# Performance work log

Measured on AMD Instinct MI355X. Metric: run time of the kernel, lower is better.

The kernel has to match this reference:

```python
import jax, jax.numpy as jnp
import numpy as np

EPS = 1e-12

def _normalize(x, axis=-1):
    # matches torch F.normalize: x / max(||x||, eps)
    n = jnp.sqrt(jnp.sum(x * x, axis=axis, keepdims=True))
    return x / jnp.maximum(n, EPS)

def setup_inputs() -> dict:
    key = jax.random.key(0)
    k1, k2, k3, k4, k5 = jax.random.split(key, 5)
    B, D, N = 65536, 512, 64
    feature = jax.random.normal(k1, (B, D), dtype=jnp.float32)
    target = jax.random.randint(k2, (B, N), 0, 2, dtype=jnp.int32)
    W = jax.random.normal(k3, (N, 2, D), dtype=jnp.float32) * 0.05
    b = jax.random.normal(k4, (N, 2), dtype=jnp.float32) * 0.01
    u = jax.random.normal(k5, (N, 2), dtype=jnp.float32)
    return {"feature": feature, "target": target, "W": W, "b": b, "u": u}

def reference(feature, target, W, b, u):
    # spectral norm, one power iteration per head (torch default n_power_iterations=1)
    v = _normalize(jnp.einsum('nod,no->nd', W, u))      # [N, D]
    u1 = _normalize(jnp.einsum('nod,nd->no', W, v))      # [N, 2]
    # u, v are buffers (no grad through them in torch)
    u_s = jax.lax.stop_gradient(u1)
    v_s = jax.lax.stop_gradient(v)
    sigma = jnp.einsum('no,nod,nd->n', u_s, W, v_s)      # [N]
    W_sn = W / sigma[:, None, None]
    # dropout in eval mode = identity; fused batched matmul over all heads
    pred = jnp.einsum('bd,nod->bno', feature, W_sn) + b[None]   # [B, N, 2]
    output = jnp.argmax(pred, axis=2)                           # [B, N]
    # CrossEntropyLoss with soft targets: class dim is dim=1 (nclass), as in torch code
    onehot = jax.nn.one_hot(target, 2, dtype=jnp.float32)       # [B, N, 2]
    logp = jax.nn.log_softmax(pred, axis=1)                     # softmax over nclass dim
    loss = jnp.mean(-jnp.sum(onehot * logp, axis=1))            # mean over B and the 2-dim
    return pred, output, loss
```

## Files before the change

### kernel.cpp

```cpp
#include <hip/hip_runtime.h>
#include <math.h>

typedef __bf16 bf16x8 __attribute__((ext_vector_type(8)));
typedef float  f32x4  __attribute__((ext_vector_type(4)));

#define BROWS 65536
#define DIM   512
#define NHEAD 64
#define NCOL  128

#define PRED_SZ  ((size_t)BROWS * NCOL)
#define ARG_BASE PRED_SZ
#define LOSS_IDX (PRED_SZ + (size_t)BROWS * NHEAD)
#define BF_OFF   ARG_BASE
#define PART_OFF (ARG_BASE + 1056 * (size_t)NHEAD)
#define FIX_ROWS 1088


__global__ __launch_bounds__(64) void spectral_kernel(
    const float* __restrict__ W, const float* __restrict__ u,
    __bf16* __restrict__ Bfrag)
{
    int n = blockIdx.x;
    int lane = threadIdx.x;

    const float* W0 = W + (size_t)n * 2 * DIM;
    const float* W1 = W0 + DIM;
    float u0 = u[2 * n], u1v = u[2 * n + 1];

    float w0[8], w1[8], vr[8];
    {
        float4 a0 = *(const float4*)(W0 + lane * 8);
        float4 a1 = *(const float4*)(W0 + lane * 8 + 4);
        float4 b0 = *(const float4*)(W1 + lane * 8);
        float4 b1 = *(const float4*)(W1 + lane * 8 + 4);
        w0[0]=a0.x; w0[1]=a0.y; w0[2]=a0.z; w0[3]=a0.w;
        w0[4]=a1.x; w0[5]=a1.y; w0[6]=a1.z; w0[7]=a1.w;
        w1[0]=b0.x; w1[1]=b0.y; w1[2]=b0.z; w1[3]=b0.w;
        w1[4]=b1.x; w1[5]=b1.y; w1[6]=b1.z; w1[7]=b1.w;
    }

    float ss = 0.f;
#pragma unroll
    for (int j = 0; j < 8; ++j) {
        vr[j] = fmaf(w0[j], u0, w1[j] * u1v);
        ss = fmaf(vr[j], vr[j], ss);
    }
#pragma unroll
    for (int m = 32; m >= 1; m >>= 1) ss += __shfl_xor(ss, m, 64);
    float inv_n = 1.f / fmaxf(sqrtf(ss), 1e-12f);

    float s0 = 0.f, s1 = 0.f;
#pragma unroll
    for (int j = 0; j < 8; ++j) {
        float v = vr[j] * inv_n;
        s0 = fmaf(w0[j], v, s0);
        s1 = fmaf(w1[j], v, s1);
    }
#pragma unroll
    for (int m = 32; m >= 1; m >>= 1) {
        s0 += __shfl_xor(s0, m, 64);
        s1 += __shfl_xor(s1, m, 64);
    }
    float nu = sqrtf(fmaf(s0, s0, s1 * s1));
    float inv_nu = 1.f / fmaxf(nu, 1e-12f);
    float sigma = fmaf(s0 * inv_nu, s0, (s1 * inv_nu) * s1);
    float inv_sigma = 1.f / sigma;

    int kc2 = lane >> 2;
    int q   = lane & 3;
#pragma unroll
    for (int o = 0; o < 2; ++o) {
        int col = 2 * n + o;
        int nt = col >> 4, cc = col & 15;
        bf16x8 hi;
#pragma unroll
        for (int j = 0; j < 8; ++j)
            hi[j] = (__bf16)((o ? w1[j] : w0[j]) * inv_sigma);
        *(bf16x8*)(Bfrag + (size_t)(kc2 * 8 + nt) * 512 + (q * 16 + cc) * 8) = hi;
    }
}

#define CVT8H(H, F0, F1) {            \
    H[0] = (__bf16)(F0).x; H[1] = (__bf16)(F0).y; \
    H[2] = (__bf16)(F0).z; H[3] = (__bf16)(F0).w; \
    H[4] = (__bf16)(F1).x; H[5] = (__bf16)(F1).y; \
    H[6] = (__bf16)(F1).z; H[7] = (__bf16)(F1).w; }

__device__ __forceinline__ void gld_lds16(const __bf16* g, __bf16* l) {
    __builtin_amdgcn_global_load_lds(
        (const __attribute__((address_space(1))) void*)g,
        (__attribute__((address_space(3))) void*)l, 16, 0, 0);
}

__global__ __launch_bounds__(1024, 4) void gemm_fused(
    const float* __restrict__ A, const int* __restrict__ target,
    const __bf16* __restrict__ Bfrag, const float* __restrict__ bias,
    float* __restrict__ pred, float* __restrict__ outArg,
    float* __restrict__ partials)
{
    __shared__ __bf16 Bs[32768];

    int tid  = threadIdx.x;
    int wave = tid >> 6;
    int lane = tid & 63;
    int q = lane >> 4;
    int c = lane & 15;
    int rowBase = blockIdx.x * 256 + wave * 16;

    f32x4 acc[8] = {};

    const float* ap = A + (size_t)(rowBase + c) * DIM + q * 8;
    float4 x0 = *(const float4*)(ap);
    float4 x1 = *(const float4*)(ap + 4);

#pragma unroll
    for (int half = 0; half < 2; ++half) {
        if (half) __syncthreads();
        {
            const __bf16* gB = Bfrag + (size_t)half * 32768
                             + (size_t)(wave * 4) * 512 + lane * 8;
            __bf16* lB = Bs + (size_t)(wave * 4) * 512;
#pragma unroll
            for (int t = 0; t < 4; ++t)
                gld_lds16(gB + t * 512, lB + t * 512);
        }
        __syncthreads();

#pragma unroll
        for (int kc = 0; kc < 8; ++kc) {
            float4 n0, n1;
            if (!(half == 1 && kc == 7)) {
                int kn = half * 256 + kc * 32 + 32;
                n0 = *(const float4*)(ap + kn);
                n1 = *(const float4*)(ap + kn + 4);
            }
            bf16x8 ah;
            CVT8H(ah, x0, x1);
#pragma unroll
            for (int nt = 0; nt < 8; ++nt) {
                bf16x8 b = *(const bf16x8*)(Bs + (size_t)(kc * 8 + nt) * 512 + lane * 8);
                acc[nt] = __builtin_amdgcn_mfma_f32_16x16x32_bf16(ah, b, acc[nt], 0, 0, 0);
            }
            if (!(half == 1 && kc == 7)) { x0 = n0; x1 = n1; }
        }
    }

    float bv[8];
#pragma unroll
    for (int nt = 0; nt < 8; ++nt) bv[nt] = bias[nt * 16 + c];

    float lp = 0.f;
    bool doA = (rowBase >= FIX_ROWS);
#pragma unroll
    for (int reg = 0; reg < 4; ++reg) {
        int row = rowBase + q * 4 + reg;
        float p[8];
#pragma unroll
        for (int nt = 0; nt < 8; ++nt) p[nt] = acc[nt][reg] + bv[nt];
#pragma unroll
        for (int nt = 0; nt < 8; ++nt)
            pred[(size_t)row * NCOL + nt * 16 + c] = p[nt];

        float M = p[0];
#pragma unroll
        for (int nt = 1; nt < 8; ++nt) M = fmaxf(M, p[nt]);
        M = fmaxf(M, __shfl_xor(M, 2, 64));
        M = fmaxf(M, __shfl_xor(M, 4, 64));
        M = fmaxf(M, __shfl_xor(M, 8, 64));
        float Mx = __shfl_xor(M, 1, 64);

        float sE = 0.f;
#pragma unroll
        for (int nt = 0; nt < 8; ++nt) sE += expf(p[nt] - M);
        sE += __shfl_xor(sE, 2, 64);
        sE += __shfl_xor(sE, 4, 64);
        sE += __shfl_xor(sE, 8, 64);
        float sX = __shfl_xor(sE, 1, 64);

        float Lown = M + logf(sE);
        float Loth = Mx + logf(sX);
        float L0 = (c & 1) ? Loth : Lown;
        float L1 = (c & 1) ? Lown : Loth;

        float pn[8];
#pragma unroll
        for (int nt = 0; nt < 8; ++nt) pn[nt] = __shfl_xor(p[nt], 1, 64);

        if ((c & 1) == 0) {
            const int* trow = target + (size_t)row * NHEAD;
            float* arow = outArg + (size_t)row * NHEAD;
#pragma unroll
            for (int nt = 0; nt < 8; ++nt) {
                int head = nt * 8 + (c >> 1);
                int t = trow[head];
                lp += t ? (L1 - pn[nt]) : (L0 - p[nt]);
                if (doA) arow[head] = (pn[nt] > p[nt]) ? 1.f : 0.f;
            }
        }
    }

#pragma unroll
    for (int m = 32; m >= 1; m >>= 1) lp += __shfl_xor(lp, m, 64);
    float* wsum = (float*)Bs;
    __syncthreads();
    if (lane == 0) wsum[wave] = lp;
    __syncthreads();
    if (tid == 0) {
        float s = 0.f;
#pragma unroll
        for (int w = 0; w < 16; ++w) s += wsum[w];
        partials[blockIdx.x] = s;
    }
}

__global__ __launch_bounds__(256) void fixup_kernel(
    const float* __restrict__ pred, const float* __restrict__ partials,
    float* __restrict__ outArg, float* __restrict__ lossOut)
{
    int tid = threadIdx.x;
    if (blockIdx.x == 0) {
        __shared__ double red[256];
        red[tid] = (double)partials[tid];
        __syncthreads();
        for (int m = 128; m >= 1; m >>= 1) {
            if (tid < m) red[tid] += red[tid + m];
            __syncthreads();
        }
        if (tid == 0) lossOut[0] = (float)(red[0] / 131072.0);
        __syncthreads();
        int row = 1056 + (tid >> 3);
        int hb = (tid & 7) * 8;
        const float* pr = pred + (size_t)row * NCOL;
        float* ar = outArg + (size_t)row * NHEAD;
#pragma unroll
        for (int h = 0; h < 8; ++h) {
            float a = pr[2 * (hb + h)], b = pr[2 * (hb + h) + 1];
            ar[hb + h] = (b > a) ? 1.f : 0.f;
        }
    } else {
        int row = (blockIdx.x - 1) * 16 + (tid >> 4);
        int hb = (tid & 15) * 4;
        const float* pr = pred + (size_t)row * NCOL;
        float* ar = outArg + (size_t)row * NHEAD;
#pragma unroll
        for (int h = 0; h < 4; ++h) {
            float a = pr[2 * (hb + h)], b = pr[2 * (hb + h) + 1];
            ar[hb + h] = (b > a) ? 1.f : 0.f;
        }
    }
}

extern "C" void kernel_launch(void* const* d_in, const int* in_sizes, int n_in,
                              void* d_out, int out_size, void* d_ws, size_t ws_size,
                              hipStream_t stream) {
    const float* feature = (const float*)d_in[0];
    const int*   target  = (const int*)d_in[1];
    const float* W       = (const float*)d_in[2];
    const float* bias    = (const float*)d_in[3];
    const float* u       = (const float*)d_in[4];

    float* out     = (float*)d_out;
    float* pred    = out;
    float* outArg  = out + ARG_BASE;
    float* lossOut = out + LOSS_IDX;
    __bf16* Bfrag  = (__bf16*)(out + BF_OFF);
    float* partial = out + PART_OFF;

    spectral_kernel<<<NHEAD, 64, 0, stream>>>(W, u, Bfrag);
    gemm_fused<<<BROWS / 256, 1024, 0, stream>>>(feature, target, Bfrag, bias,
                                                 pred, outArg, partial);
    fixup_kernel<<<67, 256, 0, stream>>>(pred, partial, outArg, lossOut);
}
```

Baseline: 243.5 us.

## Halve GEMM block size, deepen A prefetch ring, hoist target loads

The fused GEMM block shrinks from 1024 to 512 threads, covering 128 rows each, so twice as many blocks are launched and each wave loads twice as many B fragments into LDS. The single-step register prefetch of feature rows becomes a four-deep ring of float4 buffers, putting more global loads in flight ahead of the MFMAs. Target values are loaded into registers before the epilogue instead of inside the loss loop, and the partial-sum reduction now folds pairs of partials to match the doubled block count. The costs are higher register pressure and more per-block B staging traffic.

New measurement: 235.4 us. 1.03x faster.

```diff
diff --git a/kernel.cpp b/kernel.cpp
--- a/kernel.cpp
+++ b/kernel.cpp
@@ -93,7 +93,7 @@
         (__attribute__((address_space(3))) void*)l, 16, 0, 0);
 }
 
-__global__ __launch_bounds__(1024, 4) void gemm_fused(
+__global__ __launch_bounds__(512, 4) void gemm_fused(
     const float* __restrict__ A, const int* __restrict__ target,
     const __bf16* __restrict__ Bfrag, const float* __restrict__ bias,
     float* __restrict__ pred, float* __restrict__ outArg,
@@ -106,49 +106,63 @@
     int lane = tid & 63;
     int q = lane >> 4;
     int c = lane & 15;
-    int rowBase = blockIdx.x * 256 + wave * 16;
+    int rowBase = blockIdx.x * 128 + wave * 16;
 
     f32x4 acc[8] = {};
 
     const float* ap = A + (size_t)(rowBase + c) * DIM + q * 8;
-    float4 x0 = *(const float4*)(ap);
-    float4 x1 = *(const float4*)(ap + 4);
+
+    float4 buf0[4], buf1[4];
+#pragma unroll
+    for (int i = 0; i < 4; ++i) {
+        buf0[i] = *(const float4*)(ap + i * 32);
+        buf1[i] = *(const float4*)(ap + i * 32 + 4);
+    }
 
 #pragma unroll
     for (int half = 0; half < 2; ++half) {
         if (half) __syncthreads();
         {
             const __bf16* gB = Bfrag + (size_t)half * 32768
-                             + (size_t)(wave * 4) * 512 + lane * 8;
-            __bf16* lB = Bs + (size_t)(wave * 4) * 512;
-#pragma unroll
-            for (int t = 0; t < 4; ++t)
+                             + (size_t)(wave * 8) * 512 + lane * 8;
+            __bf16* lB = Bs + (size_t)(wave * 8) * 512;
+#pragma unroll
+            for (int t = 0; t < 8; ++t)
                 gld_lds16(gB + t * 512, lB + t * 512);
         }
         __syncthreads();
 
 #pragma unroll
         for (int kc = 0; kc < 8; ++kc) {
-            float4 n0, n1;
-            if (!(half == 1 && kc == 7)) {
-                int kn = half * 256 + kc * 32 + 32;
-                n0 = *(const float4*)(ap + kn);
-                n1 = *(const float4*)(ap + kn + 4);
+            int it = half * 8 + kc;
+            bf16x8 ah;
+            CVT8H(ah, buf0[it & 3], buf1[it & 3]);
+            if (it < 12) {
+                buf0[it & 3] = *(const float4*)(ap + (it + 4) * 32);
+                buf1[it & 3] = *(const float4*)(ap + (it + 4) * 32 + 4);
             }
-            bf16x8 ah;
-            CVT8H(ah, x0, x1);
 #pragma unroll
             for (int nt = 0; nt < 8; ++nt) {
                 bf16x8 b = *(const bf16x8*)(Bs + (size_t)(kc * 8 + nt) * 512 + lane * 8);
                 acc[nt] = __builtin_amdgcn_mfma_f32_16x16x32_bf16(ah, b, acc[nt], 0, 0, 0);
             }
-            if (!(half == 1 && kc == 7)) { x0 = n0; x1 = n1; }
         }
     }
 
     float bv[8];
 #pragma unroll
     for (int nt = 0; nt < 8; ++nt) bv[nt] = bias[nt * 16 + c];
+
+    bool ce = ((c & 1) == 0);
+    int tv[4][8];
+    if (ce) {
+#pragma unroll
+        for (int reg = 0; reg < 4; ++reg) {
+            const int* trow = target + (size_t)(rowBase + q * 4 + reg) * NHEAD + (c >> 1);
+#pragma unroll
+            for (int nt = 0; nt < 8; ++nt) tv[reg][nt] = trow[nt * 8];
+        }
+    }
 
     float lp = 0.f;
     bool doA = (rowBase >= FIX_ROWS);
@@ -187,15 +201,13 @@
 #pragma unroll
         for (int nt = 0; nt < 8; ++nt) pn[nt] = __shfl_xor(p[nt], 1, 64);
 
-        if ((c & 1) == 0) {
-            const int* trow = target + (size_t)row * NHEAD;
+        if (ce) {
             float* arow = outArg + (size_t)row * NHEAD;
 #pragma unroll
             for (int nt = 0; nt < 8; ++nt) {
-                int head = nt * 8 + (c >> 1);
-                int t = trow[head];
+                int t = tv[reg][nt];
                 lp += t ? (L1 - pn[nt]) : (L0 - p[nt]);
-                if (doA) arow[head] = (pn[nt] > p[nt]) ? 1.f : 0.f;
+                if (doA) arow[nt * 8 + (c >> 1)] = (pn[nt] > p[nt]) ? 1.f : 0.f;
             }
         }
     }
@@ -209,7 +221,7 @@
     if (tid == 0) {
         float s = 0.f;
 #pragma unroll
-        for (int w = 0; w < 16; ++w) s += wsum[w];
+        for (int w = 0; w < 8; ++w) s += wsum[w];
         partials[blockIdx.x] = s;
     }
 }
@@ -221,7 +233,7 @@
     int tid = threadIdx.x;
     if (blockIdx.x == 0) {
         __shared__ double red[256];
-        red[tid] = (double)partials[tid];
+        red[tid] = (double)partials[2 * tid] + (double)partials[2 * tid + 1];
         __syncthreads();
         for (int m = 128; m >= 1; m >>= 1) {
             if (tid < m) red[tid] += red[tid + m];
@@ -268,7 +280,7 @@
     float* partial = out + PART_OFF;
 
     spectral_kernel<<<NHEAD, 64, 0, stream>>>(W, u, Bfrag);
-    gemm_fused<<<BROWS / 256, 1024, 0, stream>>>(feature, target, Bfrag, bias,
-                                                 pred, outArg, partial);
+    gemm_fused<<<BROWS / 128, 512, 0, stream>>>(feature, target, Bfrag, bias,
+                                                pred, outArg, partial);
     fixup_kernel<<<67, 256, 0, stream>>>(pred, partial, outArg, lossOut);
 }
```
